# Kernel optimization log

Measured on AMD Instinct MI355X. Metric: run time of the kernel, lower is better.

The kernel has to match this reference:

```python
import jax, jax.numpy as jnp
import numpy as np
from jax import lax

EMBED = 768
D_INNER = 2 * EMBED          # expand = 2
D_STATE = 16
D_CONV = 4
DT_RANK = (EMBED + 15) // 16  # 48
FF = 3072
B, L = 2, 1024


def setup_inputs() -> dict:
    key = jax.random.key(0)
    ks = jax.random.split(key, 20)
    s = 0.02
    inp = {
        "x": jax.random.normal(ks[0], (B, L, EMBED), jnp.float32),
        # Mamba params
        "in_proj_w": jax.random.normal(ks[1], (2 * D_INNER, EMBED), jnp.float32) * s,
        "conv_w": jax.random.normal(ks[2], (D_INNER, 1, D_CONV), jnp.float32) * s,
        "conv_b": jnp.zeros((D_INNER,), jnp.float32),
        "x_proj_w": jax.random.normal(ks[3], (DT_RANK + 2 * D_STATE, D_INNER), jnp.float32) * s,
        "dt_proj_w": jax.random.normal(ks[4], (D_INNER, DT_RANK), jnp.float32) * s,
        "dt_proj_b": jax.random.normal(ks[5], (D_INNER,), jnp.float32) * s,
        "A_log": jnp.log(jnp.broadcast_to(jnp.arange(1, D_STATE + 1, dtype=jnp.float32), (D_INNER, D_STATE))),
        "D_param": jnp.ones((D_INNER,), jnp.float32),
        "out_proj_w": jax.random.normal(ks[6], (EMBED, D_INNER), jnp.float32) * s,
        # block params
        "ln1_w": jnp.ones((EMBED,), jnp.float32), "ln1_b": jnp.zeros((EMBED,), jnp.float32),
        "ln2_w": jnp.ones((EMBED,), jnp.float32), "ln2_b": jnp.zeros((EMBED,), jnp.float32),
        "ffn_w1": jax.random.normal(ks[7], (FF, EMBED), jnp.float32) * s,
        "ffn_b1": jnp.zeros((FF,), jnp.float32),
        "ffn_w2": jax.random.normal(ks[8], (EMBED, FF), jnp.float32) * s,
        "ffn_b2": jnp.zeros((EMBED,), jnp.float32),
    }
    return inp


def _layernorm(x, w, b, eps=1e-5):
    mu = jnp.mean(x, -1, keepdims=True)
    var = jnp.mean((x - mu) ** 2, -1, keepdims=True)
    return (x - mu) * lax.rsqrt(var + eps) * w + b


def _mamba(x, in_proj_w, conv_w, conv_b, x_proj_w, dt_proj_w, dt_proj_b,
           A_log, D_param, out_proj_w):
    # x: [B, L, E]
    xz = jnp.einsum('ble,de->bld', x, in_proj_w)          # [B,L,2*Di]
    xin, z = jnp.split(xz, 2, axis=-1)                    # [B,L,Di] each
    # causal depthwise conv over time
    xc = lax.conv_general_dilated(
        xin.transpose(0, 2, 1), conv_w, window_strides=(1,),
        padding=[(D_CONV - 1, 0)], feature_group_count=D_INNER,
        dimension_numbers=('NCH', 'OIH', 'NCH'))
    xc = (xc + conv_b[None, :, None]).transpose(0, 2, 1)  # [B,L,Di]
    xc = jax.nn.silu(xc)
    # input-dependent SSM params
    x_dbl = jnp.einsum('bld,rd->blr', xc, x_proj_w)       # [B,L,dt_rank+2n]
    dt, Bm, Cm = jnp.split(x_dbl, [DT_RANK, DT_RANK + D_STATE], axis=-1)
    delta = jax.nn.softplus(jnp.einsum('blr,dr->bld', dt, dt_proj_w) + dt_proj_b)
    A = -jnp.exp(A_log)                                   # [Di, n]
    deltaA = jnp.exp(jnp.einsum('bld,dn->bldn', delta, A))
    deltaBu = jnp.einsum('bld,bln,bld->bldn', delta, Bm, xc)

    def step(h, xs):
        dA, dBu, Ct = xs                                  # [B,Di,n],[B,Di,n],[B,n]
        h = dA * h + dBu
        y = jnp.einsum('bdn,bn->bd', h, Ct)
        return h, y

    h0 = jnp.zeros((x.shape[0], D_INNER, D_STATE), x.dtype)
    _, ys = lax.scan(step, h0, (deltaA.transpose(1, 0, 2, 3),
                                deltaBu.transpose(1, 0, 2, 3),
                                Cm.transpose(1, 0, 2)))
    y = ys.transpose(1, 0, 2)                             # [B,L,Di]
    y = y + xc * D_param
    y = y * jax.nn.silu(z)
    return jnp.einsum('bld,ed->ble', y, out_proj_w)


def reference(x, in_proj_w, conv_w, conv_b, x_proj_w, dt_proj_w, dt_proj_b,
              A_log, D_param, out_proj_w, ln1_w, ln1_b, ln2_w, ln2_b,
              ffn_w1, ffn_b1, ffn_w2, ffn_b2):
    # dropout is identity in eval mode
    h = _mamba(x, in_proj_w, conv_w, conv_b, x_proj_w, dt_proj_w, dt_proj_b,
               A_log, D_param, out_proj_w)
    x1 = _layernorm(h + x, ln1_w, ln1_b)
    f = jnp.einsum('ble,fe->blf', x1, ffn_w1) + ffn_b1
    f = jax.nn.gelu(f)
    f = jnp.einsum('blf,ef->ble', f, ffn_w2) + ffn_b2
    return _layernorm(f + x1, ln2_w, ln2_b)
```

## Files before the change

### kernel.cpp

```cpp
#include <hip/hip_runtime.h>
#include <math.h>

#define EMBED 768
#define DI 1536
#define DSTATE 16
#define DCONV 4
#define DTRANK 48
#define FF 3072
#define BATCH 2
#define SEQ 1024
#define NROWS (BATCH*SEQ)
#define TCH 32
#define NCH (SEQ/TCH)
#define DBLK 64

typedef __bf16 bf16x8 __attribute__((ext_vector_type(8)));
typedef float f32x4 __attribute__((ext_vector_type(4)));
typedef unsigned int u32x4 __attribute__((ext_vector_type(4)));

static __device__ __forceinline__ unsigned short f2b(float f) {
    union { float f; unsigned u; } v; v.f = f;
    unsigned r = v.u + 0x7FFFu + ((v.u >> 16) & 1u);
    return (unsigned short)(r >> 16);
}
static __device__ __forceinline__ float b2f(unsigned short s) {
    union { unsigned u; float f; } v; v.u = ((unsigned)s) << 16;
    return v.f;
}

#define GLOAD_LDS16(g, l) __builtin_amdgcn_global_load_lds( \
    (const __attribute__((address_space(1))) void*)(g), \
    (__attribute__((address_space(3))) void*)(l), 16, 0, 0)

template<int EPI, int KSPLIT>
__global__ __launch_bounds__(256)
void gemm_sk(const unsigned short* __restrict__ A,
             const unsigned short* __restrict__ W,
             float* __restrict__ C, unsigned short* __restrict__ Cb,
             float* __restrict__ part,
             int M, int N, int K,
             const float* __restrict__ bias)
{
    __shared__ alignas(16) unsigned short As[128 * 32];
    __shared__ alignas(16) unsigned short Ws[64 * 32];
    const int tid  = threadIdx.x;
    const int lane = tid & 63, wave = tid >> 6;
    const int bm = blockIdx.y * 128, bn = blockIdx.x * 64;
    const int kc = K / KSPLIT;
    const int kz = blockIdx.z * kc;
    const int ln = lane & 15, lg = lane >> 4;

    f32x4 acc[2][4];
    #pragma unroll
    for (int i = 0; i < 2; ++i)
        #pragma unroll
        for (int j = 0; j < 4; ++j)
            acc[i][j] = (f32x4){0.f, 0.f, 0.f, 0.f};

    const int ra = tid >> 2, ca = tid & 3;
    const int cs = (ca * 8) ^ ((ra & 3) << 3);
    const unsigned short* gA0 = A + (size_t)(bm + ra) * K + kz + cs;
    const unsigned short* gA1 = A + (size_t)(bm + ra + 64) * K + kz + cs;
    const unsigned short* gW  = W + (size_t)(bn + ra) * K + kz + cs;
    unsigned short* ldsA0 = As + wave * 512;
    unsigned short* ldsA1 = As + 2048 + wave * 512;
    unsigned short* ldsW  = Ws + wave * 512;

    for (int k0 = 0; k0 < kc; k0 += 32) {
        GLOAD_LDS16(gA0 + k0, ldsA0);
        GLOAD_LDS16(gA1 + k0, ldsA1);
        GLOAD_LDS16(gW  + k0, ldsW);
        __syncthreads();
        bf16x8 af[2], wf[4];
        #pragma unroll
        for (int i = 0; i < 2; ++i) {
            int row = wave * 32 + i * 16 + ln;
            af[i] = *reinterpret_cast<const bf16x8*>(
                &As[row * 32 + ((lg * 8) ^ ((row & 3) << 3))]);
        }
        #pragma unroll
        for (int j = 0; j < 4; ++j) {
            int row = j * 16 + ln;
            wf[j] = *reinterpret_cast<const bf16x8*>(
                &Ws[row * 32 + ((lg * 8) ^ ((row & 3) << 3))]);
        }
        #pragma unroll
        for (int i = 0; i < 2; ++i)
            #pragma unroll
            for (int j = 0; j < 4; ++j)
                acc[i][j] = __builtin_amdgcn_mfma_f32_16x16x32_bf16(af[i], wf[j], acc[i][j], 0, 0, 0);
        __syncthreads();
    }

    if constexpr (KSPLIT > 1) {
        float* pb = part + (size_t)blockIdx.z * M * N;
        #pragma unroll
        for (int i = 0; i < 2; ++i)
            #pragma unroll
            for (int j = 0; j < 4; ++j) {
                int col = bn + j * 16 + ln;
                #pragma unroll
                for (int rr = 0; rr < 4; ++rr) {
                    int row = bm + wave * 32 + i * 16 + lg * 4 + rr;
                    pb[(size_t)row * N + col] = acc[i][j][rr];
                }
            }
    } else {
        #pragma unroll
        for (int i = 0; i < 2; ++i)
            #pragma unroll
            for (int j = 0; j < 4; ++j) {
                int col = bn + j * 16 + ln;
                #pragma unroll
                for (int rr = 0; rr < 4; ++rr) {
                    int row = bm + wave * 32 + i * 16 + lg * 4 + rr;
                    float v = acc[i][j][rr];
                    size_t o = (size_t)row * N + col;
                    if (EPI == 1) {
                        v += bias[col];
                        C[o] = (v > 20.f) ? v : log1pf(expf(v));
                    } else if (EPI == 3) {
                        v += bias[col];
                        float t = 0.7978845608028654f * (v + 0.044715f * v * v * v);
                        Cb[o] = f2b(0.5f * v * (1.f + tanhf(t)));
                    } else if (EPI == 5) {
                        if (col < DI) C[(size_t)row * DI + col] = v;
                        else          Cb[(size_t)row * DI + col - DI] = f2b(v);
                    } else {
                        C[o] = v;
                    }
                }
            }
    }
}

template<int KS, int BIAS>
__global__ __launch_bounds__(256)
void reduce_ln(const float* __restrict__ part, const float* __restrict__ resid,
               const float* __restrict__ bias,
               const float* __restrict__ w, const float* __restrict__ bb,
               float* __restrict__ out, unsigned short* __restrict__ outb)
{
    const int row = blockIdx.x;
    const size_t ro = (size_t)row * EMBED;
    const int i0 = threadIdx.x, i1 = i0 + 256, i2 = i0 + 512;
    float v0 = 0.f, v1 = 0.f, v2 = 0.f;
    #pragma unroll
    for (int z = 0; z < KS; ++z) {
        const float* p = part + (size_t)z * NROWS * EMBED + ro;
        v0 += p[i0]; v1 += p[i1]; v2 += p[i2];
    }
    if (BIAS) { v0 += bias[i0]; v1 += bias[i1]; v2 += bias[i2]; }
    v0 += resid[ro + i0]; v1 += resid[ro + i1]; v2 += resid[ro + i2];

    float s  = v0 + v1 + v2;
    float s2 = v0 * v0 + v1 * v1 + v2 * v2;
    #pragma unroll
    for (int m = 1; m < 64; m <<= 1) {
        s  += __shfl_xor(s,  m);
        s2 += __shfl_xor(s2, m);
    }
    __shared__ float sh1[4], sh2[4];
    int wv = threadIdx.x >> 6;
    if ((threadIdx.x & 63) == 0) { sh1[wv] = s; sh2[wv] = s2; }
    __syncthreads();
    float S1 = sh1[0] + sh1[1] + sh1[2] + sh1[3];
    float S2 = sh2[0] + sh2[1] + sh2[2] + sh2[3];
    float mu  = S1 * (1.f / EMBED);
    float var = S2 * (1.f / EMBED) - mu * mu;
    float rs  = rsqrtf(var + 1e-5f);
    float o0 = (v0 - mu) * rs * w[i0] + bb[i0];
    float o1 = (v1 - mu) * rs * w[i1] + bb[i1];
    float o2 = (v2 - mu) * rs * w[i2] + bb[i2];
    out[ro + i0] = o0; out[ro + i1] = o1; out[ro + i2] = o2;
    if (outb) {
        outb[ro + i0] = f2b(o0); outb[ro + i1] = f2b(o1); outb[ro + i2] = f2b(o2);
    }
}

__global__ __launch_bounds__(256)
void xproj_mfma(const unsigned short* __restrict__ A,
                const unsigned short* __restrict__ W,
                float* __restrict__ part)
{
    const int mt = blockIdx.x, s = blockIdx.y;
    const int lane = threadIdx.x & 63, wave = threadIdx.x >> 6;
    const int ln = lane & 15, lg = lane >> 4;
    const int row0 = mt * 128 + wave * 32;
    const int kb = s * 192;
    f32x4 acc[2][5];
    #pragma unroll
    for (int i = 0; i < 2; ++i)
        #pragma unroll
        for (int j = 0; j < 5; ++j)
            acc[i][j] = (f32x4){0.f, 0.f, 0.f, 0.f};

    for (int kk = 0; kk < 192; kk += 32) {
        const int k = kb + kk + lg * 8;
        bf16x8 af[2], wf[5];
        af[0] = *reinterpret_cast<const bf16x8*>(A + (size_t)(row0 + ln) * DI + k);
        af[1] = *reinterpret_cast<const bf16x8*>(A + (size_t)(row0 + 16 + ln) * DI + k);
        #pragma unroll
        for (int j = 0; j < 5; ++j)
            wf[j] = *reinterpret_cast<const bf16x8*>(W + (size_t)(j * 16 + ln) * DI + k);
        #pragma unroll
        for (int i = 0; i < 2; ++i)
            #pragma unroll
            for (int j = 0; j < 5; ++j)
                acc[i][j] = __builtin_amdgcn_mfma_f32_16x16x32_bf16(af[i], wf[j], acc[i][j], 0, 0, 0);
    }
    float* pb = part + (size_t)s * NROWS * 80;
    #pragma unroll
    for (int i = 0; i < 2; ++i)
        #pragma unroll
        for (int j = 0; j < 5; ++j)
            #pragma unroll
            for (int rr = 0; rr < 4; ++rr) {
                int row = row0 + i * 16 + lg * 4 + rr;
                int col = j * 16 + ln;
                pb[(size_t)row * 80 + col] = acc[i][j][rr];
            }
}

__global__ __launch_bounds__(256)
void xproj_reduce(const float* __restrict__ part, float* __restrict__ xdbl,
                  unsigned short* __restrict__ xdblb)
{
    int idx = blockIdx.x * 256 + threadIdx.x;
    float sum = 0.f;
    #pragma unroll
    for (int s = 0; s < 8; ++s) sum += part[(size_t)s * NROWS * 80 + idx];
    xdbl[idx] = sum;
    int col = idx % 80, row = idx / 80;
    if (col < 48)      xdblb[row * 64 + col] = f2b(sum);
    else if (col < 64) xdblb[row * 64 + col] = 0;
}

__global__ __launch_bounds__(256)
void cvt7_k(const float* __restrict__ x,  const float* __restrict__ w1,
            const float* __restrict__ w2, const float* __restrict__ w3,
            const float* __restrict__ w4, const float* __restrict__ w5,
            const float* __restrict__ w6,
            unsigned short* __restrict__ xb,  unsigned short* __restrict__ w1b,
            unsigned short* __restrict__ w2b, unsigned short* __restrict__ w3b,
            unsigned short* __restrict__ w4b, unsigned short* __restrict__ w5b,
            unsigned short* __restrict__ w6b)
{
    size_t i4 = ((size_t)blockIdx.x * 256 + threadIdx.x) * 4;
    if (i4 >= 9953280u) {
        int off = (int)(i4 - 9953280u);
        if (off >= 98304) return;
        int row = off >> 6, colb = off & 63;
        ushort4 u = {0, 0, 0, 0};
        if (colb < 48) {
            float4 v = *reinterpret_cast<const float4*>(w6 + row * 48 + colb);
            u.x = f2b(v.x); u.y = f2b(v.y); u.z = f2b(v.z); u.w = f2b(v.w);
        }
        *reinterpret_cast<ushort4*>(w6b + off) = u;
        return;
    }
    const float* src; unsigned short* dst; size_t off;
    if      (i4 < 1572864u) { src = x;  dst = xb;  off = i4; }
    else if (i4 < 3932160u) { src = w1; dst = w1b; off = i4 - 1572864u; }
    else if (i4 < 5111808u) { src = w2; dst = w2b; off = i4 - 3932160u; }
    else if (i4 < 7471104u) { src = w3; dst = w3b; off = i4 - 5111808u; }
    else if (i4 < 9830400u) { src = w4; dst = w4b; off = i4 - 7471104u; }
    else                    { src = w5; dst = w5b; off = i4 - 9830400u; }
    float4 v = *reinterpret_cast<const float4*>(src + off);
    ushort4 u;
    u.x = f2b(v.x); u.y = f2b(v.y); u.z = f2b(v.z); u.w = f2b(v.w);
    *reinterpret_cast<ushort4*>(dst + off) = u;
}

__global__ __launch_bounds__(256)
void conv_silu_k(const float* __restrict__ xin, const float* __restrict__ cw,
                 const float* __restrict__ cb, float* __restrict__ xc,
                 unsigned short* __restrict__ xcb)
{
    int q = blockIdx.x * 256 + threadIdx.x;
    int d4 = (q * 4) % DI;
    int bt = (q * 4) / DI;
    int t  = bt % SEQ;
    const float* base = xin + (size_t)bt * DI + d4;
    float4 s3 = *reinterpret_cast<const float4*>(base);
    float4 acc = *reinterpret_cast<const float4*>(cb + d4);
    float4 wv0 = *reinterpret_cast<const float4*>(cw + (d4 + 0) * 4);
    float4 wv1 = *reinterpret_cast<const float4*>(cw + (d4 + 1) * 4);
    float4 wv2 = *reinterpret_cast<const float4*>(cw + (d4 + 2) * 4);
    float4 wv3 = *reinterpret_cast<const float4*>(cw + (d4 + 3) * 4);
    acc.x += wv0.w * s3.x; acc.y += wv1.w * s3.y; acc.z += wv2.w * s3.z; acc.w += wv3.w * s3.w;
    if (t >= 1) {
        float4 s = *reinterpret_cast<const float4*>(base - DI);
        acc.x += wv0.z * s.x; acc.y += wv1.z * s.y; acc.z += wv2.z * s.z; acc.w += wv3.z * s.w;
    }
    if (t >= 2) {
        float4 s = *reinterpret_cast<const float4*>(base - 2 * DI);
        acc.x += wv0.y * s.x; acc.y += wv1.y * s.y; acc.z += wv2.y * s.z; acc.w += wv3.y * s.w;
    }
    if (t >= 3) {
        float4 s = *reinterpret_cast<const float4*>(base - 3 * DI);
        acc.x += wv0.x * s.x; acc.y += wv1.x * s.y; acc.z += wv2.x * s.z; acc.w += wv3.x * s.w;
    }
    float4 v;
    v.x = acc.x / (1.f + __expf(-acc.x));
    v.y = acc.y / (1.f + __expf(-acc.y));
    v.z = acc.z / (1.f + __expf(-acc.z));
    v.w = acc.w / (1.f + __expf(-acc.w));
    size_t o = (size_t)bt * DI + d4;
    *reinterpret_cast<float4*>(xc + o) = v;
    ushort4 u; u.x = f2b(v.x); u.y = f2b(v.y); u.z = f2b(v.z); u.w = f2b(v.w);
    *reinterpret_cast<ushort4*>(xcb + o) = u;
}

__global__ __launch_bounds__(256)
void scan2_a(const float* __restrict__ delta, const float* __restrict__ xc,
             const float* __restrict__ xdbl,  const float* __restrict__ A_log,
             float* __restrict__ hfin, float* __restrict__ aprod)
{
    const int d0 = blockIdx.x * DBLK, ch = blockIdx.y, b = blockIdx.z;
    const int t0 = ch * TCH;
    __shared__ float del_s[TCH][DBLK + 4];
    __shared__ float xc_s[TCH][DBLK + 4];
    __shared__ float b_s[TCH][20];
    const int tid = threadIdx.x;
    {
        const int c4 = tid & 15, tr = tid >> 4;
        #pragma unroll
        for (int p = 0; p < 2; ++p) {
            int t = p * 16 + tr;
            size_t rowo = (size_t)(b * SEQ + t0 + t);
            *reinterpret_cast<float4*>(&del_s[t][c4 * 4]) =
                *reinterpret_cast<const float4*>(&delta[rowo * DI + d0 + c4 * 4]);
            *reinterpret_cast<float4*>(&xc_s[t][c4 * 4]) =
                *reinterpret_cast<const float4*>(&xc[rowo * DI + d0 + c4 * 4]);
        }
        const int cbq = tid & 3, tb = tid >> 2;
        if (tb < TCH) {
            size_t rowo = (size_t)(b * SEQ + t0 + tb);
            *reinterpret_cast<float4*>(&b_s[tb][cbq * 4]) =
                *reinterpret_cast<const float4*>(&xdbl[rowo * 80 + DTRANK + cbq * 4]);
        }
    }
    __syncthreads();
    const int lane = tid & 63, wave = tid >> 6;
    const int wd = wave * 16 + (lane >> 2);
    const int d = d0 + wd;
    const int nq = (lane & 3) * 4;
    float4 Av = *reinterpret_cast<const float4*>(&A_log[d * DSTATE + nq]);
    const float A0 = -__expf(Av.x), A1 = -__expf(Av.y), A2 = -__expf(Av.z), A3 = -__expf(Av.w);
    float h0_ = 0.f, h1_ = 0.f, h2_ = 0.f, h3_ = 0.f;
    float p0 = 1.f, p1 = 1.f, p2 = 1.f, p3 = 1.f;
    #pragma unroll 4
    for (int t = 0; t < TCH; ++t) {
        float dl = del_s[t][wd];
        float u  = dl * xc_s[t][wd];
        float4 bq = *reinterpret_cast<const float4*>(&b_s[t][nq]);
        float e0 = __expf(dl * A0), e1 = __expf(dl * A1);
        float e2 = __expf(dl * A2), e3 = __expf(dl * A3);
        h0_ = e0 * h0_ + u * bq.x; p0 *= e0;
        h1_ = e1 * h1_ + u * bq.y; p1 *= e1;
        h2_ = e2 * h2_ + u * bq.z; p2 *= e2;
        h3_ = e3 * h3_ + u * bq.w; p3 *= e3;
    }
    size_t o = ((size_t)((b * NCH + ch) * DI) + d) * DSTATE + nq;
    *reinterpret_cast<float4*>(&hfin[o])  = (float4){h0_, h1_, h2_, h3_};
    *reinterpret_cast<float4*>(&aprod[o]) = (float4){p0, p1, p2, p3};
}

__global__ __launch_bounds__(256)
void scan2_b(const float* __restrict__ hfin, const float* __restrict__ aprod,
             float* __restrict__ h0)
{
    int idx = blockIdx.x * 256 + threadIdx.x;
    int nq = (idx & 3) * 4;
    int d  = (idx >> 2) % DI;
    int b  = (idx >> 2) / DI;
    float4 h = {0.f, 0.f, 0.f, 0.f};
    #pragma unroll
    for (int ch = 0; ch < NCH; ++ch) {
        size_t o = ((size_t)((b * NCH + ch) * DI) + d) * DSTATE + nq;
        *reinterpret_cast<float4*>(&h0[o]) = h;
        float4 a = *reinterpret_cast<const float4*>(&aprod[o]);
        float4 f = *reinterpret_cast<const float4*>(&hfin[o]);
        h.x = a.x * h.x + f.x; h.y = a.y * h.y + f.y;
        h.z = a.z * h.z + f.z; h.w = a.w * h.w + f.w;
    }
}

__global__ __launch_bounds__(256)
void scan2_c(const float* __restrict__ delta, const float* __restrict__ xc,
             const float* __restrict__ xdbl,  const float* __restrict__ A_log,
             const float* __restrict__ Dp,    const unsigned short* __restrict__ zb,
             const float* __restrict__ h0,
             unsigned short* __restrict__ yb)
{
    const int d0 = blockIdx.x * DBLK, ch = blockIdx.y, b = blockIdx.z;
    const int t0 = ch * TCH;
    __shared__ float del_s[TCH][DBLK + 4];
    __shared__ float xc_s[TCH][DBLK + 4];
    __shared__ float b_s[TCH][20];
    __shared__ float c_s[TCH][20];
    __shared__ unsigned short z_s[TCH][DBLK + 8];
    const int tid = threadIdx.x;
    {
        const int c4 = tid & 15, tr = tid >> 4;
        #pragma unroll
        for (int p = 0; p < 2; ++p) {
            int t = p * 16 + tr;
            size_t rowo = (size_t)(b * SEQ + t0 + t);
            *reinterpret_cast<float4*>(&del_s[t][c4 * 4]) =
                *reinterpret_cast<const float4*>(&delta[rowo * DI + d0 + c4 * 4]);
            *reinterpret_cast<float4*>(&xc_s[t][c4 * 4]) =
                *reinterpret_cast<const float4*>(&xc[rowo * DI + d0 + c4 * 4]);
        }
        const int cbq = tid & 3, tb = tid >> 2;
        if (tb < TCH) {
            size_t rowo = (size_t)(b * SEQ + t0 + tb);
            *reinterpret_cast<float4*>(&b_s[tb][cbq * 4]) =
                *reinterpret_cast<const float4*>(&xdbl[rowo * 80 + DTRANK + cbq * 4]);
        } else {
            size_t rowo = (size_t)(b * SEQ + t0 + tb - TCH);
            *reinterpret_cast<float4*>(&c_s[tb - TCH][cbq * 4]) =
                *reinterpret_cast<const float4*>(&xdbl[rowo * 80 + DTRANK + DSTATE + cbq * 4]);
        }
        const int cz = tid & 7, tz = tid >> 3;
        size_t rz = (size_t)(b * SEQ + t0 + tz);
        *reinterpret_cast<u32x4*>(&z_s[tz][cz * 8]) =
            *reinterpret_cast<const u32x4*>(&zb[rz * DI + d0 + cz * 8]);
    }
    __syncthreads();
    const int lane = tid & 63, wave = tid >> 6;
    const int wd = wave * 16 + (lane >> 2);
    const int d = d0 + wd;
    const int nq = (lane & 3) * 4;
    float4 Av = *reinterpret_cast<const float4*>(&A_log[d * DSTATE + nq]);
    const float A0 = -__expf(Av.x), A1 = -__expf(Av.y), A2 = -__expf(Av.z), A3 = -__expf(Av.w);
    const float Dd = Dp[d];
    float4 h = *reinterpret_cast<const float4*>(
        &h0[((size_t)((b * NCH + ch) * DI) + d) * DSTATE + nq]);
    unsigned short* yrow = yb + (size_t)(b * SEQ + t0) * DI + d;
    #pragma unroll 4
    for (int t = 0; t < TCH; ++t) {
        float dl = del_s[t][wd];
        float xv = xc_s[t][wd];
        float u  = dl * xv;
        float4 bq = *reinterpret_cast<const float4*>(&b_s[t][nq]);
        float4 cq = *reinterpret_cast<const float4*>(&c_s[t][nq]);
        float e0 = __expf(dl * A0), e1 = __expf(dl * A1);
        float e2 = __expf(dl * A2), e3 = __expf(dl * A3);
        h.x = e0 * h.x + u * bq.x;
        h.y = e1 * h.y + u * bq.y;
        h.z = e2 * h.z + u * bq.z;
        h.w = e3 * h.w + u * bq.w;
        float py = h.x * cq.x + h.y * cq.y + h.z * cq.z + h.w * cq.w;
        py += __shfl_xor(py, 1);
        py += __shfl_xor(py, 2);
        if ((lane & 3) == 0) {
            float yv = py + xv * Dd;
            float zv = b2f(z_s[t][wd]);
            yv *= zv / (1.f + __expf(-zv));
            yrow[(size_t)t * DI] = f2b(yv);
        }
    }
}

extern "C" void kernel_launch(void* const* d_in, const int* in_sizes, int n_in,
                              void* d_out, int out_size, void* d_ws, size_t ws_size,
                              hipStream_t stream)
{
    const float* x         = (const float*)d_in[0];
    const float* in_proj_w = (const float*)d_in[1];
    const float* conv_w    = (const float*)d_in[2];
    const float* conv_b    = (const float*)d_in[3];
    const float* x_proj_w  = (const float*)d_in[4];
    const float* dt_proj_w = (const float*)d_in[5];
    const float* dt_proj_b = (const float*)d_in[6];
    const float* A_log     = (const float*)d_in[7];
    const float* D_param   = (const float*)d_in[8];
    const float* out_proj_w= (const float*)d_in[9];
    const float* ln1_w     = (const float*)d_in[10];
    const float* ln1_b     = (const float*)d_in[11];
    const float* ln2_w     = (const float*)d_in[12];
    const float* ln2_b     = (const float*)d_in[13];
    const float* ffn_w1    = (const float*)d_in[14];
    const float* ffn_b1    = (const float*)d_in[15];
    const float* ffn_w2    = (const float*)d_in[16];
    const float* ffn_b2    = (const float*)d_in[17];
    float* out = (float*)d_out;

    char* Wp = (char*)d_ws;
    float*          xin   = (float*)         (Wp + 0);
    unsigned short* zbuf  = (unsigned short*)(Wp + 12582912);
    float*          xc    = (float*)         (Wp + 18874368);
    float*          xdbl  = (float*)         (Wp + 31457280);
    float*          delta = (float*)         (Wp + 32112640);
    unsigned short* ybb   = (unsigned short*)(Wp + 44695552);
    unsigned short* xb    = (unsigned short*)(Wp + 58851328);
    unsigned short* wib   = (unsigned short*)(Wp + 61997056);
    unsigned short* wob   = (unsigned short*)(Wp + 66715648);
    unsigned short* wf1b  = (unsigned short*)(Wp + 69074944);
    unsigned short* wf2b  = (unsigned short*)(Wp + 73793536);
    unsigned short* fbf   = (unsigned short*)(Wp + 0);
    float*          x1    = (float*)         (Wp + 32112640);
    unsigned short* x1b   = (unsigned short*)(Wp + 58851328);
    float*          part  = (float*)         (Wp + 0);
    unsigned short* xdblb = (unsigned short*)(Wp + 5242880);
    unsigned short* xcb   = (unsigned short*)(Wp + 58851328);
    unsigned short* xpwb  = (unsigned short*)(Wp + 50987008);
    unsigned short* wdtb  = (unsigned short*)(Wp + 51232768);
    float*          hfin  = (float*)         (Wp + 0);
    float*          aprod = (float*)         (Wp + 6291456);
    float*          h0    = (float*)         (Wp + 50987008);
    float*          part_op = (float*)       (Wp + 0);
    float*          part_f2 = (float*)       (Wp + 38404096);

    dim3 blk(256);

    cvt7_k<<<9816, blk, 0, stream>>>(x, in_proj_w, out_proj_w, ffn_w1, ffn_w2, x_proj_w,
                                     dt_proj_w, xb, wib, wob, wf1b, wf2b, xpwb, wdtb);

    gemm_sk<5, 1><<<dim3(48, 16, 1), blk, 0, stream>>>(xb, wib, xin, zbuf, nullptr,
                                                       NROWS, 2 * DI, EMBED, nullptr);

    conv_silu_k<<<(BATCH * SEQ * DI) / 1024, blk, 0, stream>>>(xin, conv_w, conv_b, xc, xcb);

    xproj_mfma<<<dim3(16, 8), blk, 0, stream>>>(xcb, xpwb, part);
    xproj_reduce<<<640, blk, 0, stream>>>(part, xdbl, xdblb);

    gemm_sk<1, 1><<<dim3(24, 16, 1), blk, 0, stream>>>(xdblb, wdtb, delta, nullptr, nullptr,
                                                       NROWS, DI, 64, dt_proj_b);

    scan2_a<<<dim3(DI / DBLK, NCH, BATCH), blk, 0, stream>>>(delta, xc, xdbl, A_log, hfin, aprod);
    scan2_b<<<48, blk, 0, stream>>>(hfin, aprod, h0);
    scan2_c<<<dim3(DI / DBLK, NCH, BATCH), blk, 0, stream>>>(delta, xc, xdbl, A_log, D_param,
                                                             zbuf, h0, ybb);

    gemm_sk<0, 4><<<dim3(12, 16, 4), blk, 0, stream>>>(ybb, wob, nullptr, nullptr, part_op,
                                                       NROWS, EMBED, DI, nullptr);
    reduce_ln<4, 0><<<NROWS, blk, 0, stream>>>(part_op, x, nullptr, ln1_w, ln1_b, x1, x1b);

    gemm_sk<3, 1><<<dim3(48, 16, 1), blk, 0, stream>>>(x1b, wf1b, nullptr, fbf, nullptr,
                                                       NROWS, FF, EMBED, ffn_b1);

    gemm_sk<0, 4><<<dim3(12, 16, 4), blk, 0, stream>>>(fbf, wf2b, nullptr, nullptr, part_f2,
                                                       NROWS, EMBED, FF, nullptr);
    reduce_ln<4, 1><<<NROWS, blk, 0, stream>>>(part_f2, x1, ffn_b2, ln2_w, ln2_b, out, nullptr);
}
```

Before: 208.5 us.

## Double-buffer GEMM LDS tiles and store in_proj output as bf16

The GEMM now double-buffers its LDS tiles. The global-to-LDS load of the next K slice is issued before computing on the current one, which drops one barrier per iteration and aims to overlap memory latency with MFMA. The in_proj GEMM writes the whole xz result as bf16 instead of fp32 x plus bf16 z, and the conv and scan kernels read that interleaved buffer. This halves the traffic for the x half at the cost of bf16 rounding before the convolution. The workspace layout is reassigned with non-overlapping regions, which doubles LDS use per block.

```diff
diff --git a/kernel.cpp b/kernel.cpp
--- a/kernel.cpp
+++ b/kernel.cpp
@@ -41,8 +41,8 @@
              int M, int N, int K,
              const float* __restrict__ bias)
 {
-    __shared__ alignas(16) unsigned short As[128 * 32];
-    __shared__ alignas(16) unsigned short Ws[64 * 32];
+    __shared__ alignas(16) unsigned short As[2][128 * 32];
+    __shared__ alignas(16) unsigned short Ws[2][64 * 32];
     const int tid  = threadIdx.x;
     const int lane = tid & 63, wave = tid >> 6;
     const int bm = blockIdx.y * 128, bn = blockIdx.x * 64;
@@ -62,27 +62,30 @@
     const unsigned short* gA0 = A + (size_t)(bm + ra) * K + kz + cs;
     const unsigned short* gA1 = A + (size_t)(bm + ra + 64) * K + kz + cs;
     const unsigned short* gW  = W + (size_t)(bn + ra) * K + kz + cs;
-    unsigned short* ldsA0 = As + wave * 512;
-    unsigned short* ldsA1 = As + 2048 + wave * 512;
-    unsigned short* ldsW  = Ws + wave * 512;
-
+
+#define STAGE(bf, kk) do { \
+        GLOAD_LDS16(gA0 + (kk), &As[bf][wave * 512]); \
+        GLOAD_LDS16(gA1 + (kk), &As[bf][2048 + wave * 512]); \
+        GLOAD_LDS16(gW  + (kk), &Ws[bf][wave * 512]); \
+    } while (0)
+
+    STAGE(0, 0);
+    __syncthreads();
+    int buf = 0;
     for (int k0 = 0; k0 < kc; k0 += 32) {
-        GLOAD_LDS16(gA0 + k0, ldsA0);
-        GLOAD_LDS16(gA1 + k0, ldsA1);
-        GLOAD_LDS16(gW  + k0, ldsW);
-        __syncthreads();
+        if (k0 + 32 < kc) STAGE(buf ^ 1, k0 + 32);
         bf16x8 af[2], wf[4];
         #pragma unroll
         for (int i = 0; i < 2; ++i) {
             int row = wave * 32 + i * 16 + ln;
             af[i] = *reinterpret_cast<const bf16x8*>(
-                &As[row * 32 + ((lg * 8) ^ ((row & 3) << 3))]);
+                &As[buf][row * 32 + ((lg * 8) ^ ((row & 3) << 3))]);
         }
         #pragma unroll
         for (int j = 0; j < 4; ++j) {
             int row = j * 16 + ln;
             wf[j] = *reinterpret_cast<const bf16x8*>(
-                &Ws[row * 32 + ((lg * 8) ^ ((row & 3) << 3))]);
+                &Ws[buf][row * 32 + ((lg * 8) ^ ((row & 3) << 3))]);
         }
         #pragma unroll
         for (int i = 0; i < 2; ++i)
@@ -90,7 +93,9 @@
             for (int j = 0; j < 4; ++j)
                 acc[i][j] = __builtin_amdgcn_mfma_f32_16x16x32_bf16(af[i], wf[j], acc[i][j], 0, 0, 0);
         __syncthreads();
-    }
+        buf ^= 1;
+    }
+#undef STAGE
 
     if constexpr (KSPLIT > 1) {
         float* pb = part + (size_t)blockIdx.z * M * N;
@@ -123,9 +128,8 @@
                         v += bias[col];
                         float t = 0.7978845608028654f * (v + 0.044715f * v * v * v);
                         Cb[o] = f2b(0.5f * v * (1.f + tanhf(t)));
-                    } else if (EPI == 5) {
-                        if (col < DI) C[(size_t)row * DI + col] = v;
-                        else          Cb[(size_t)row * DI + col - DI] = f2b(v);
+                    } else if (EPI == 6) {
+                        Cb[o] = f2b(v);
                     } else {
                         C[o] = v;
                     }
@@ -273,7 +277,7 @@
 }
 
 __global__ __launch_bounds__(256)
-void conv_silu_k(const float* __restrict__ xin, const float* __restrict__ cw,
+void conv_silu_k(const unsigned short* __restrict__ xz, const float* __restrict__ cw,
                  const float* __restrict__ cb, float* __restrict__ xc,
                  unsigned short* __restrict__ xcb)
 {
@@ -281,25 +285,31 @@
     int d4 = (q * 4) % DI;
     int bt = (q * 4) / DI;
     int t  = bt % SEQ;
-    const float* base = xin + (size_t)bt * DI + d4;
-    float4 s3 = *reinterpret_cast<const float4*>(base);
+    const unsigned short* base = xz + (size_t)bt * (2 * DI) + d4;
     float4 acc = *reinterpret_cast<const float4*>(cb + d4);
     float4 wv0 = *reinterpret_cast<const float4*>(cw + (d4 + 0) * 4);
     float4 wv1 = *reinterpret_cast<const float4*>(cw + (d4 + 1) * 4);
     float4 wv2 = *reinterpret_cast<const float4*>(cw + (d4 + 2) * 4);
     float4 wv3 = *reinterpret_cast<const float4*>(cw + (d4 + 3) * 4);
-    acc.x += wv0.w * s3.x; acc.y += wv1.w * s3.y; acc.z += wv2.w * s3.z; acc.w += wv3.w * s3.w;
+    {
+        ushort4 r = *reinterpret_cast<const ushort4*>(base);
+        acc.x += wv0.w * b2f(r.x); acc.y += wv1.w * b2f(r.y);
+        acc.z += wv2.w * b2f(r.z); acc.w += wv3.w * b2f(r.w);
+    }
     if (t >= 1) {
-        float4 s = *reinterpret_cast<const float4*>(base - DI);
-        acc.x += wv0.z * s.x; acc.y += wv1.z * s.y; acc.z += wv2.z * s.z; acc.w += wv3.z * s.w;
+        ushort4 r = *reinterpret_cast<const ushort4*>(base - 2 * DI);
+        acc.x += wv0.z * b2f(r.x); acc.y += wv1.z * b2f(r.y);
+        acc.z += wv2.z * b2f(r.z); acc.w += wv3.z * b2f(r.w);
     }
     if (t >= 2) {
-        float4 s = *reinterpret_cast<const float4*>(base - 2 * DI);
-        acc.x += wv0.y * s.x; acc.y += wv1.y * s.y; acc.z += wv2.y * s.z; acc.w += wv3.y * s.w;
+        ushort4 r = *reinterpret_cast<const ushort4*>(base - 4 * DI);
+        acc.x += wv0.y * b2f(r.x); acc.y += wv1.y * b2f(r.y);
+        acc.z += wv2.y * b2f(r.z); acc.w += wv3.y * b2f(r.w);
     }
     if (t >= 3) {
-        float4 s = *reinterpret_cast<const float4*>(base - 3 * DI);
-        acc.x += wv0.x * s.x; acc.y += wv1.x * s.y; acc.z += wv2.x * s.z; acc.w += wv3.x * s.w;
+        ushort4 r = *reinterpret_cast<const ushort4*>(base - 6 * DI);
+        acc.x += wv0.x * b2f(r.x); acc.y += wv1.x * b2f(r.y);
+        acc.z += wv2.x * b2f(r.z); acc.w += wv3.x * b2f(r.w);
     }
     float4 v;
     v.x = acc.x / (1.f + __expf(-acc.x));
@@ -390,7 +400,7 @@
 __global__ __launch_bounds__(256)
 void scan2_c(const float* __restrict__ delta, const float* __restrict__ xc,
              const float* __restrict__ xdbl,  const float* __restrict__ A_log,
-             const float* __restrict__ Dp,    const unsigned short* __restrict__ zb,
+             const float* __restrict__ Dp,    const unsigned short* __restrict__ xz,
              const float* __restrict__ h0,
              unsigned short* __restrict__ yb)
 {
@@ -426,7 +436,7 @@
         const int cz = tid & 7, tz = tid >> 3;
         size_t rz = (size_t)(b * SEQ + t0 + tz);
         *reinterpret_cast<u32x4*>(&z_s[tz][cz * 8]) =
-            *reinterpret_cast<const u32x4*>(&zb[rz * DI + d0 + cz * 8]);
+            *reinterpret_cast<const u32x4*>(&xz[rz * (2 * DI) + DI + d0 + cz * 8]);
     }
     __syncthreads();
     const int lane = tid & 63, wave = tid >> 6;
@@ -489,40 +499,41 @@
     float* out = (float*)d_out;
 
     char* Wp = (char*)d_ws;
-    float*          xin   = (float*)         (Wp + 0);
-    unsigned short* zbuf  = (unsigned short*)(Wp + 12582912);
-    float*          xc    = (float*)         (Wp + 18874368);
-    float*          xdbl  = (float*)         (Wp + 31457280);
-    float*          delta = (float*)         (Wp + 32112640);
-    unsigned short* ybb   = (unsigned short*)(Wp + 44695552);
-    unsigned short* xb    = (unsigned short*)(Wp + 58851328);
-    unsigned short* wib   = (unsigned short*)(Wp + 61997056);
-    unsigned short* wob   = (unsigned short*)(Wp + 66715648);
-    unsigned short* wf1b  = (unsigned short*)(Wp + 69074944);
-    unsigned short* wf2b  = (unsigned short*)(Wp + 73793536);
-    unsigned short* fbf   = (unsigned short*)(Wp + 0);
-    float*          x1    = (float*)         (Wp + 32112640);
-    unsigned short* x1b   = (unsigned short*)(Wp + 58851328);
-    float*          part  = (float*)         (Wp + 0);
-    unsigned short* xdblb = (unsigned short*)(Wp + 5242880);
-    unsigned short* xcb   = (unsigned short*)(Wp + 58851328);
-    unsigned short* xpwb  = (unsigned short*)(Wp + 50987008);
-    unsigned short* wdtb  = (unsigned short*)(Wp + 51232768);
-    float*          hfin  = (float*)         (Wp + 0);
-    float*          aprod = (float*)         (Wp + 6291456);
-    float*          h0    = (float*)         (Wp + 50987008);
-    float*          part_op = (float*)       (Wp + 0);
-    float*          part_f2 = (float*)       (Wp + 38404096);
+    #define MB(n) ((size_t)(n) * 1048576)
+    unsigned short* xzb   = (unsigned short*)(Wp + 0);
+    float*          xc    = (float*)         (Wp + MB(16));
+    unsigned short* xcb   = (unsigned short*)(Wp + MB(30));
+    float*          xdbl  = (float*)         (Wp + MB(38));
+    unsigned short* xdblb = (unsigned short*)(Wp + MB(40));
+    float*          delta = (float*)         (Wp + MB(42));
+    unsigned short* ybb   = (unsigned short*)(Wp + MB(56));
+    float*          hfin  = (float*)         (Wp + MB(66));
+    float*          aprod = (float*)         (Wp + MB(76));
+    float*          h0    = (float*)         (Wp + MB(86));
+    unsigned short* xb    = (unsigned short*)(Wp + MB(92));
+    unsigned short* wib   = (unsigned short*)(Wp + MB(96));
+    unsigned short* wob   = (unsigned short*)(Wp + MB(101));
+    unsigned short* wf1b  = (unsigned short*)(Wp + MB(104));
+    unsigned short* wf2b  = (unsigned short*)(Wp + MB(109));
+    unsigned short* xpwb  = (unsigned short*)(Wp + MB(114));
+    unsigned short* wdtb  = (unsigned short*)(Wp + MB(115));
+    float*          part  = (float*)         (Wp + MB(116));
+    float*          part_op = (float*)       (Wp + MB(122));
+    float*          part_f2 = (float*)       (Wp + MB(148));
+    float*          x1    = (float*)         (Wp + MB(174));
+    unsigned short* x1b   = (unsigned short*)(Wp + MB(181));
+    unsigned short* fbf   = (unsigned short*)(Wp + MB(185));
+    #undef MB
 
     dim3 blk(256);
 
     cvt7_k<<<9816, blk, 0, stream>>>(x, in_proj_w, out_proj_w, ffn_w1, ffn_w2, x_proj_w,
                                      dt_proj_w, xb, wib, wob, wf1b, wf2b, xpwb, wdtb);
 
-    gemm_sk<5, 1><<<dim3(48, 16, 1), blk, 0, stream>>>(xb, wib, xin, zbuf, nullptr,
+    gemm_sk<6, 1><<<dim3(48, 16, 1), blk, 0, stream>>>(xb, wib, nullptr, xzb, nullptr,
                                                        NROWS, 2 * DI, EMBED, nullptr);
 
-    conv_silu_k<<<(BATCH * SEQ * DI) / 1024, blk, 0, stream>>>(xin, conv_w, conv_b, xc, xcb);
+    conv_silu_k<<<(BATCH * SEQ * DI) / 1024, blk, 0, stream>>>(xzb, conv_w, conv_b, xc, xcb);
 
     xproj_mfma<<<dim3(16, 8), blk, 0, stream>>>(xcb, xpwb, part);
     xproj_reduce<<<640, blk, 0, stream>>>(part, xdbl, xdblb);
@@ -533,7 +544,7 @@
     scan2_a<<<dim3(DI / DBLK, NCH, BATCH), blk, 0, stream>>>(delta, xc, xdbl, A_log, hfin, aprod);
     scan2_b<<<48, blk, 0, stream>>>(hfin, aprod, h0);
     scan2_c<<<dim3(DI / DBLK, NCH, BATCH), blk, 0, stream>>>(delta, xc, xdbl, A_log, D_param,
-                                                             zbuf, h0, ybb);
+                                                             xzb, h0, ybb);
 
     gemm_sk<0, 4><<<dim3(12, 16, 4), blk, 0, stream>>>(ybb, wob, nullptr, nullptr, part_op,
                                                        NROWS, EMBED, DI, nullptr);
```

Measured after the change: 205.5 us. About the same (-1.4%).
